# Kernel optimization log

Hardware: AMD Instinct MI355X
Metric: run time of the kernel (lower is better)

Reference implementation:

```python
import jax, jax.numpy as jnp
import numpy as np

EMB = 1024
HEADS = 16
HEAD_DIM = EMB // HEADS

def setup_inputs() -> dict:
    key = jax.random.key(0)
    ks = jax.random.split(key, 12)
    s = 0.02
    x = jax.random.normal(ks[0], (2, 2048, EMB), dtype=jnp.float32)
    return {
        "x": x,
        "wq": jax.random.normal(ks[1], (EMB, EMB), jnp.float32) * s,
        "bq": jnp.zeros((EMB,), jnp.float32),
        "wk": jax.random.normal(ks[2], (EMB, EMB), jnp.float32) * s,
        "bk": jnp.zeros((EMB,), jnp.float32),
        "wv": jax.random.normal(ks[3], (EMB, EMB), jnp.float32) * s,
        "bv": jnp.zeros((EMB,), jnp.float32),
        "wo": jax.random.normal(ks[4], (EMB, EMB), jnp.float32) * s,
        "bo": jnp.zeros((EMB,), jnp.float32),
        "gamma": jnp.ones((EMB,), jnp.float32),
        "beta": jnp.zeros((EMB,), jnp.float32),
    }

def _layernorm(x, gamma, beta, eps=1e-5):
    mu = jnp.mean(x, axis=-1, keepdims=True)
    var = jnp.mean(jnp.square(x - mu), axis=-1, keepdims=True)
    return (x - mu) * jax.lax.rsqrt(var + eps) * gamma + beta

def reference(x, wq, bq, wk, bk, wv, bv, wo, bo, gamma, beta):
    B, T, D = x.shape
    H, d_k = HEADS, HEAD_DIM
    # Linear(y = x W^T + b), then split heads
    q = (x @ wq.T + bq).reshape(B, T, H, d_k)
    k = (x @ wk.T + bk).reshape(B, T, H, d_k)
    v = (x @ wv.T + bv).reshape(B, T, H, d_k)
    scores = jnp.einsum('bthd,bshd->bhts', q, k) / jnp.sqrt(jnp.float32(d_k))
    attn = jax.nn.softmax(scores, axis=-1)  # dropout is identity in eval mode
    out = jnp.einsum('bhts,bshd->bthd', attn, v).reshape(B, T, D)
    out = out @ wo.T + bo
    return _layernorm(x + out, gamma, beta)
```

## Files before the change

### kernel.cpp

```cpp
#include <hip/hip_runtime.h>
#include <stdint.h>
#include <stddef.h>


typedef __bf16 bf16_t;
typedef bf16_t bf16x8 __attribute__((ext_vector_type(8)));
typedef float f32x16 __attribute__((ext_vector_type(16)));
typedef uint16_t u16x8 __attribute__((ext_vector_type(8)));

#define MFMA32(a, b, c) __builtin_amdgcn_mfma_f32_32x32x16_bf16((a), (b), (c), 0, 0, 0)

__device__ __forceinline__ uint16_t f2bf(float f) {
  __bf16 h = (__bf16)f;
  return *(uint16_t*)&h;
}

__device__ __forceinline__ void gload16(const void* g, void* l) {
  __builtin_amdgcn_global_load_lds((const __attribute__((address_space(1))) void*)g,
                                   (__attribute__((address_space(3))) void*)l,
                                   16, 0, 0);
}

__global__ __launch_bounds__(256) void cvt_all(
    const float* __restrict__ x, const float* __restrict__ wq,
    const float* __restrict__ wk, const float* __restrict__ wv,
    const float* __restrict__ wo, uint16_t* __restrict__ xb,
    uint16_t* __restrict__ wqb, uint16_t* __restrict__ wkb,
    uint16_t* __restrict__ wvb, uint16_t* __restrict__ wob) {
  const int gid = blockIdx.x * 256 + threadIdx.x;
  const float* src; uint16_t* dst; int off;
  if (gid < 1048576) {
    src = x; dst = xb; off = gid;
  } else {
    const int t = gid - 1048576;
    off = t & 262143;
    switch (t >> 18) {
      case 0: src = wq; dst = wqb; break;
      case 1: src = wk; dst = wkb; break;
      case 2: src = wv; dst = wvb; break;
      default: src = wo; dst = wob; break;
    }
  }
  const float4 f = ((const float4*)src)[off];
  uint64_t p = (uint64_t)f2bf(f.x) | ((uint64_t)f2bf(f.y) << 16) |
               ((uint64_t)f2bf(f.z) << 32) | ((uint64_t)f2bf(f.w) << 48);
  ((uint64_t*)dst)[off] = p;
}

template <bool OUT_BF16>
__device__ __forceinline__ void gemm128(const uint16_t* __restrict__ A,
                                        const uint16_t* __restrict__ Bt,
                                        const float* __restrict__ bias,
                                        float oscale,
                                        uint16_t* __restrict__ outb,
                                        float* __restrict__ outf) {
  __shared__ uint16_t sA[2][128 * 32];
  __shared__ uint16_t sB[2][128 * 32];
  const int tid = threadIdx.x;
  const int lane = tid & 63, w = tid >> 6;
  const int l31 = lane & 31, half = lane >> 5;
  const int m0 = blockIdx.y * 128, n0 = blockIdx.x * 128;
  const int wm = (w >> 1) * 64, wn = (w & 1) * 64;

  const int ch0 = tid, ch1 = tid + 256;
  const int r0 = ch0 >> 2, g0 = (((ch0 & 3) ^ (r0 & 3)) << 3);
  const int r1 = ch1 >> 2, g1 = (((ch1 & 3) ^ (r1 & 3)) << 3);
  const uint16_t* a0 = A + (size_t)(m0 + r0) * 1024 + g0;
  const uint16_t* a1 = A + (size_t)(m0 + r1) * 1024 + g1;
  const uint16_t* b0 = Bt + (size_t)(n0 + r0) * 1024 + g0;
  const uint16_t* b1 = Bt + (size_t)(n0 + r1) * 1024 + g1;

  gload16(a0, &sA[0][ch0 * 8]);
  gload16(a1, &sA[0][ch1 * 8]);
  gload16(b0, &sB[0][ch0 * 8]);
  gload16(b1, &sB[0][ch1 * 8]);

  f32x16 acc[2][2] = {};

  for (int kt = 0; kt < 32; ++kt) {
    __syncthreads();
    const int cur = kt & 1;
    if (kt < 31) {
      const int ko = (kt + 1) * 32;
      const int nxt = cur ^ 1;
      gload16(a0 + ko, &sA[nxt][ch0 * 8]);
      gload16(a1 + ko, &sA[nxt][ch1 * 8]);
      gload16(b0 + ko, &sB[nxt][ch0 * 8]);
      gload16(b1 + ko, &sB[nxt][ch1 * 8]);
    }
#pragma unroll
    for (int s = 0; s < 2; ++s) {
      const int c = s * 2 + half;
      bf16x8 af[2], bfr[2];
#pragma unroll
      for (int i = 0; i < 2; ++i) {
        const int arow = wm + i * 32 + l31;
        af[i] = *(const bf16x8*)&sA[cur][arow * 32 + ((c ^ (arow & 3)) << 3)];
      }
#pragma unroll
      for (int j = 0; j < 2; ++j) {
        const int brow = wn + j * 32 + l31;
        bfr[j] = *(const bf16x8*)&sB[cur][brow * 32 + ((c ^ (brow & 3)) << 3)];
      }
#pragma unroll
      for (int i = 0; i < 2; ++i)
#pragma unroll
        for (int j = 0; j < 2; ++j) acc[i][j] = MFMA32(af[i], bfr[j], acc[i][j]);
    }
  }

#pragma unroll
  for (int i = 0; i < 2; ++i) {
#pragma unroll
    for (int j = 0; j < 2; ++j) {
      const int gn = n0 + wn + j * 32 + l31;
      const float bv = bias[gn];
#pragma unroll
      for (int reg = 0; reg < 16; ++reg) {
        const int gm = m0 + wm + i * 32 + (reg & 3) + 8 * (reg >> 2) + 4 * half;
        const float v = (acc[i][j][reg] + bv) * oscale;
        const size_t idx = (size_t)gm * 1024 + gn;
        if constexpr (OUT_BF16) outb[idx] = f2bf(v);
        else outf[idx] = v;
      }
    }
  }
}

#define QSCALE 0.18033688011112042f

__global__ __launch_bounds__(256) void qkv_gemm(
    const uint16_t* __restrict__ xb, const uint16_t* __restrict__ wqb,
    const uint16_t* __restrict__ wkb, const uint16_t* __restrict__ wvb,
    const float* __restrict__ bq, const float* __restrict__ bk,
    const float* __restrict__ bv, uint16_t* __restrict__ qb,
    uint16_t* __restrict__ kb, uint16_t* __restrict__ vb) {
  const uint16_t* Bt; const float* bias; uint16_t* out; float sc;
  if (blockIdx.z == 0)      { Bt = wqb; bias = bq; out = qb; sc = QSCALE; }
  else if (blockIdx.z == 1) { Bt = wkb; bias = bk; out = kb; sc = 1.f; }
  else                      { Bt = wvb; bias = bv; out = vb; sc = 1.f; }
  gemm128<true>(xb, Bt, bias, sc, out, nullptr);
}

__global__ __launch_bounds__(256) void o_gemm(const uint16_t* __restrict__ ab,
                                              const uint16_t* __restrict__ wob,
                                              const float* __restrict__ bo,
                                              float* __restrict__ y) {
  gemm128<false>(ab, wob, bo, 1.f, nullptr, y);
}

__global__ __launch_bounds__(256) void v_trans(const uint16_t* __restrict__ vb,
                                               uint16_t* __restrict__ vbT) {
  __shared__ uint16_t sT[64 * 136];
  const int tid = threadIdx.x;
  const int t0 = blockIdx.x * 128;
  const int h = blockIdx.y, b = blockIdx.z;
#pragma unroll
  for (int c = 0; c < 4; ++c) {
    const int idx = c * 256 + tid;
    const int t = idx >> 3, d8 = (idx & 7) * 8;
    u16x8 v = *(const u16x8*)&vb[(size_t)(b * 2048 + t0 + t) * 1024 + h * 64 + d8];
#pragma unroll
    for (int e = 0; e < 8; ++e) sT[(d8 + e) * 136 + t] = v[e];
  }
  __syncthreads();
  const size_t obase = ((size_t)(b * 16 + h) * 64) * 2048 + t0;
#pragma unroll
  for (int c = 0; c < 4; ++c) {
    const int idx = c * 256 + tid;
    const int d = idx >> 4, t8 = (idx & 15) * 8;
    const int tb = t8 & ~15;
    const int add4 = (t8 & 8) ? 4 : 0;
    u16x8 v;
#pragma unroll
    for (int e = 0; e < 8; ++e)
      v[e] = sT[d * 136 + tb + ((e & 3) + ((e >> 2) << 3)) + add4];
    *(u16x8*)&vbT[obase + (size_t)d * 2048 + t8] = v;
  }
}

__global__ __launch_bounds__(512, 4) void attn(const uint16_t* __restrict__ qb,
                                               const uint16_t* __restrict__ kb,
                                               const uint16_t* __restrict__ vbT,
                                               uint16_t* __restrict__ ab) {
  __shared__ __align__(16) uint16_t smem[32768];
  uint16_t* sK = smem;
  uint16_t* sV = smem + 16384;
  const int tid = threadIdx.x;
  const int lane = tid & 63, w = tid >> 6;
  const int l31 = lane & 31, half = lane >> 5;
  const int rg = w & 3, sh = w >> 2;
  const int hb = blockIdx.x;
  const int h = hb & 15, b = hb >> 4;
  const int q0 = blockIdx.y * 128;
  const size_t qkbase = (size_t)b * 2048 * 1024 + (size_t)h * 64;
  const size_t vtbase = (size_t)hb * 64 * 2048;

  const int ch0 = tid, ch1 = tid + 512;
  const int kr0 = ch0 >> 3, kg0 = (((ch0 & 7) ^ (kr0 & 7)) << 3);
  const int kr1 = ch1 >> 3, kg1 = (((ch1 & 7) ^ (kr1 & 7)) << 3);
  const int vr0 = ch0 >> 4, vg0 = (((ch0 & 15) ^ (vr0 & 15)) << 3);
  const int vr1 = ch1 >> 4, vg1 = (((ch1 & 15) ^ (vr1 & 15)) << 3);
  const uint16_t* k0 = kb + qkbase + (size_t)kr0 * 1024 + kg0;
  const uint16_t* k1 = kb + qkbase + (size_t)kr1 * 1024 + kg1;
  const uint16_t* v0 = vbT + vtbase + (size_t)vr0 * 2048 + vg0;
  const uint16_t* v1 = vbT + vtbase + (size_t)vr1 * 2048 + vg1;

  gload16(k0, sK + ch0 * 8);
  gload16(k1, sK + ch1 * 8);
  gload16(v0, sV + ch0 * 8);
  gload16(v1, sV + ch1 * 8);

  bf16x8 qa[4];
  {
    const uint16_t* qrow =
        qb + qkbase + (size_t)(q0 + rg * 32 + l31) * 1024 + half * 8;
#pragma unroll
    for (int s4 = 0; s4 < 4; ++s4) qa[s4] = *(const bf16x8*)(qrow + s4 * 16);
  }

  f32x16 acc_o[2] = {};
  float li = 0.f;

  for (int kt = 0; kt < 16; ++kt) {
    __syncthreads();
    const int cur = kt & 1;
    if (kt < 15) {
      const size_t soK = (size_t)(kt + 1) * 128 * 1024;
      const int soV = (kt + 1) * 128;
      const int nxt = cur ^ 1;
      gload16(k0 + soK, sK + nxt * 8192 + ch0 * 8);
      gload16(k1 + soK, sK + nxt * 8192 + ch1 * 8);
      gload16(v0 + soV, sV + nxt * 8192 + ch0 * 8);
      gload16(v1 + soV, sV + nxt * 8192 + ch1 * 8);
    }
    const uint16_t* sKc = sK + cur * 8192;
    const uint16_t* sVc = sV + cur * 8192;

#pragma unroll
    for (int mblk = 0; mblk < 2; ++mblk) {
      f32x16 accs = {};
#pragma unroll
      for (int s4 = 0; s4 < 4; ++s4) {
        const int c = s4 * 2 + half;
        const int srow = sh * 64 + mblk * 32 + l31;
        const bf16x8 kk =
            *(const bf16x8*)&sKc[srow * 64 + ((c ^ (srow & 7)) << 3)];
        accs = MFMA32(kk, qa[s4], accs);
      }
      bf16x8 bp0, bp1;
#pragma unroll
      for (int reg = 0; reg < 8; ++reg) {
        const float p = __builtin_amdgcn_exp2f(accs[reg]);
        li += p;
        bp0[reg] = (__bf16)p;
      }
#pragma unroll
      for (int reg = 8; reg < 16; ++reg) {
        const float p = __builtin_amdgcn_exp2f(accs[reg]);
        li += p;
        bp1[reg - 8] = (__bf16)p;
      }
#pragma unroll
      for (int t = 0; t < 2; ++t) {
        const bf16x8 bp = t ? bp1 : bp0;
        const int cc = sh * 8 + mblk * 4 + t * 2 + half;
#pragma unroll
        for (int md = 0; md < 2; ++md) {
          const int vrow = md * 32 + l31;
          const bf16x8 vv =
              *(const bf16x8*)&sVc[vrow * 128 + ((cc ^ (vrow & 15)) << 3)];
          acc_o[md] = MFMA32(vv, bp, acc_o[md]);
        }
      }
    }
  }

  __syncthreads();
  float* ep = (float*)smem;
  float* epl = (float*)(smem + 16384);
  if (sh == 1) {
#pragma unroll
    for (int md = 0; md < 2; ++md)
#pragma unroll
      for (int reg = 0; reg < 16; ++reg)
        ep[((rg * 2 + md) * 16 + reg) * 64 + lane] = acc_o[md][reg];
    epl[rg * 64 + lane] = li;
  }
  __syncthreads();
  if (sh == 0) {
#pragma unroll
    for (int md = 0; md < 2; ++md)
#pragma unroll
      for (int reg = 0; reg < 16; ++reg)
        acc_o[md][reg] += ep[((rg * 2 + md) * 16 + reg) * 64 + lane];
    li += epl[rg * 64 + lane];
    li += __shfl_xor(li, 32);
    const float inv = 1.f / li;
    const int row = q0 + rg * 32 + l31;
    uint16_t* const obase = ab + (size_t)(b * 2048 + row) * 1024 + h * 64;
#pragma unroll
    for (int md = 0; md < 2; ++md)
#pragma unroll
      for (int g = 0; g < 4; ++g) {
        uint64_t pk = 0;
#pragma unroll
        for (int e = 0; e < 4; ++e)
          pk |= (uint64_t)f2bf(acc_o[md][g * 4 + e] * inv) << (16 * e);
        *(uint64_t*)(obase + md * 32 + g * 8 + half * 4) = pk;
      }
  }
}

__global__ __launch_bounds__(256) void resid_ln(const float* __restrict__ x,
                                                const float* __restrict__ y,
                                                const float* __restrict__ gamma,
                                                const float* __restrict__ beta,
                                                float* __restrict__ out) {
  const int row = blockIdx.x, tid = threadIdx.x;
  const size_t base = (size_t)row * 1024 + tid * 4;
  const float4 xv = *(const float4*)(x + base);
  const float4 yv = *(const float4*)(y + base);
  const float a = xv.x + yv.x, b2 = xv.y + yv.y, c = xv.z + yv.z, d = xv.w + yv.w;
  float s = a + b2 + c + d;
#pragma unroll
  for (int o = 1; o < 64; o <<= 1) s += __shfl_xor(s, o);
  __shared__ float red[4];
  const int w = tid >> 6;
  if ((tid & 63) == 0) red[w] = s;
  __syncthreads();
  const float mu = (red[0] + red[1] + red[2] + red[3]) * (1.f / 1024.f);
  const float da = a - mu, db = b2 - mu, dc = c - mu, dd = d - mu;
  float sq = da * da + db * db + dc * dc + dd * dd;
#pragma unroll
  for (int o = 1; o < 64; o <<= 1) sq += __shfl_xor(sq, o);
  __syncthreads();
  if ((tid & 63) == 0) red[w] = sq;
  __syncthreads();
  const float var = (red[0] + red[1] + red[2] + red[3]) * (1.f / 1024.f);
  const float rs = rsqrtf(var + 1e-5f);
  const float4 g = *(const float4*)(gamma + tid * 4);
  const float4 bt = *(const float4*)(beta + tid * 4);
  float4 o4;
  o4.x = da * rs * g.x + bt.x;
  o4.y = db * rs * g.y + bt.y;
  o4.z = dc * rs * g.z + bt.z;
  o4.w = dd * rs * g.w + bt.w;
  *(float4*)(out + base) = o4;
}

extern "C" void kernel_launch(void* const* d_in, const int* in_sizes, int n_in,
                              void* d_out, int out_size, void* d_ws, size_t ws_size,
                              hipStream_t stream) {
  const float* x     = (const float*)d_in[0];
  const float* wq    = (const float*)d_in[1];
  const float* bq    = (const float*)d_in[2];
  const float* wk    = (const float*)d_in[3];
  const float* bk    = (const float*)d_in[4];
  const float* wv    = (const float*)d_in[5];
  const float* bv    = (const float*)d_in[6];
  const float* wo    = (const float*)d_in[7];
  const float* bo    = (const float*)d_in[8];
  const float* gamma = (const float*)d_in[9];
  const float* beta  = (const float*)d_in[10];
  float* out = (float*)d_out;
  char* ws = (char*)d_ws;
  const size_t MB = 1024 * 1024;
  uint16_t* xb  = (uint16_t*)(ws);
  uint16_t* ab  = xb;
  uint16_t* wqb = (uint16_t*)(ws + 8 * MB);
  uint16_t* wkb = (uint16_t*)(ws + 10 * MB);
  uint16_t* wvb = (uint16_t*)(ws + 12 * MB);
  uint16_t* wob = (uint16_t*)(ws + 14 * MB);
  uint16_t* qb  = (uint16_t*)(ws + 16 * MB);
  uint16_t* kb  = (uint16_t*)(ws + 24 * MB);
  uint16_t* vb  = (uint16_t*)(ws + 32 * MB);
  uint16_t* vbT = (uint16_t*)(ws + 40 * MB);
  float*    y   = (float*)(ws + 16 * MB);

  cvt_all<<<8192, 256, 0, stream>>>(x, wq, wk, wv, wo, xb, wqb, wkb, wvb, wob);
  qkv_gemm<<<dim3(8, 32, 3), 256, 0, stream>>>(xb, wqb, wkb, wvb, bq, bk, bv, qb, kb, vb);
  v_trans<<<dim3(16, 16, 2), 256, 0, stream>>>(vb, vbT);
  attn<<<dim3(32, 16), 512, 0, stream>>>(qb, kb, vbT, ab);
  o_gemm<<<dim3(8, 32), 256, 0, stream>>>(ab, wob, bo, y);
  resid_ln<<<4096, 256, 0, stream>>>(x, y, gamma, beta, out);
}
```

Baseline: 207.9 us.

## Compute V transposed directly in QKV GEMM and use one-wave-per-row layernorm

The V projection is now computed as Wv·x^T inside the QKV GEMM, so its output lands directly in the permuted, transposed layout the attention kernel expects. This removes the separate v_trans kernel and its extra read and write of V. The residual layernorm also changes to process one row per wavefront with 4 rows per block, which drops the LDS reductions and block barriers. The transposed epilogue writes scattered 2-byte stores along rows, which may coalesce poorly.

```diff
diff --git a/kernel.cpp b/kernel.cpp
--- a/kernel.cpp
+++ b/kernel.cpp
@@ -47,19 +47,18 @@
   ((uint64_t*)dst)[off] = p;
 }
 
-template <bool OUT_BF16>
 __device__ __forceinline__ void gemm128(const uint16_t* __restrict__ A,
                                         const uint16_t* __restrict__ Bt,
                                         const float* __restrict__ bias,
                                         float oscale,
                                         uint16_t* __restrict__ outb,
-                                        float* __restrict__ outf) {
+                                        float* __restrict__ outf,
+                                        int m0, int n0, int mode) {
   __shared__ uint16_t sA[2][128 * 32];
   __shared__ uint16_t sB[2][128 * 32];
   const int tid = threadIdx.x;
   const int lane = tid & 63, w = tid >> 6;
   const int l31 = lane & 31, half = lane >> 5;
-  const int m0 = blockIdx.y * 128, n0 = blockIdx.x * 128;
   const int wm = (w >> 1) * 64, wn = (w & 1) * 64;
 
   const int ch0 = tid, ch1 = tid + 256;
@@ -109,19 +108,37 @@
     }
   }
 
-#pragma unroll
-  for (int i = 0; i < 2; ++i) {
-#pragma unroll
-    for (int j = 0; j < 2; ++j) {
-      const int gn = n0 + wn + j * 32 + l31;
-      const float bv = bias[gn];
-#pragma unroll
-      for (int reg = 0; reg < 16; ++reg) {
-        const int gm = m0 + wm + i * 32 + (reg & 3) + 8 * (reg >> 2) + 4 * half;
-        const float v = (acc[i][j][reg] + bv) * oscale;
-        const size_t idx = (size_t)gm * 1024 + gn;
-        if constexpr (OUT_BF16) outb[idx] = f2bf(v);
-        else outf[idx] = v;
+  if (mode == 2) {
+#pragma unroll
+    for (int i = 0; i < 2; ++i) {
+#pragma unroll
+      for (int j = 0; j < 2; ++j) {
+        const int gn = n0 + wn + j * 32 + l31;
+        const int bb = gn >> 11, t2 = gn & 2047;
+        const int ts = (t2 & ~12) | ((t2 & 4) << 1) | ((t2 & 8) >> 1);
+#pragma unroll
+        for (int reg = 0; reg < 16; ++reg) {
+          const int gm = m0 + wm + i * 32 + (reg & 3) + 8 * (reg >> 2) + 4 * half;
+          const float v = acc[i][j][reg] + bias[gm];
+          outb[((size_t)(bb * 1024 + gm)) * 2048 + ts] = f2bf(v);
+        }
+      }
+    }
+  } else {
+#pragma unroll
+    for (int i = 0; i < 2; ++i) {
+#pragma unroll
+      for (int j = 0; j < 2; ++j) {
+        const int gn = n0 + wn + j * 32 + l31;
+        const float bv = bias[gn];
+#pragma unroll
+        for (int reg = 0; reg < 16; ++reg) {
+          const int gm = m0 + wm + i * 32 + (reg & 3) + 8 * (reg >> 2) + 4 * half;
+          const float v = (acc[i][j][reg] + bv) * oscale;
+          const size_t idx = (size_t)gm * 1024 + gn;
+          if (mode == 0) outb[idx] = f2bf(v);
+          else outf[idx] = v;
+        }
       }
     }
   }
@@ -134,49 +151,27 @@
     const uint16_t* __restrict__ wkb, const uint16_t* __restrict__ wvb,
     const float* __restrict__ bq, const float* __restrict__ bk,
     const float* __restrict__ bv, uint16_t* __restrict__ qb,
-    uint16_t* __restrict__ kb, uint16_t* __restrict__ vb) {
-  const uint16_t* Bt; const float* bias; uint16_t* out; float sc;
-  if (blockIdx.z == 0)      { Bt = wqb; bias = bq; out = qb; sc = QSCALE; }
-  else if (blockIdx.z == 1) { Bt = wkb; bias = bk; out = kb; sc = 1.f; }
-  else                      { Bt = wvb; bias = bv; out = vb; sc = 1.f; }
-  gemm128<true>(xb, Bt, bias, sc, out, nullptr);
+    uint16_t* __restrict__ kb, uint16_t* __restrict__ vbT) {
+  const uint16_t *Aa, *Bb; const float* bias; uint16_t* out; float sc;
+  int m0, n0, mode;
+  if (blockIdx.z == 0) {
+    Aa = xb; Bb = wqb; bias = bq; out = qb; sc = QSCALE;
+    m0 = blockIdx.y * 128; n0 = blockIdx.x * 128; mode = 0;
+  } else if (blockIdx.z == 1) {
+    Aa = xb; Bb = wkb; bias = bk; out = kb; sc = 1.f;
+    m0 = blockIdx.y * 128; n0 = blockIdx.x * 128; mode = 0;
+  } else {
+    Aa = wvb; Bb = xb; bias = bv; out = vbT; sc = 1.f;
+    m0 = blockIdx.x * 128; n0 = blockIdx.y * 128; mode = 2;
+  }
+  gemm128(Aa, Bb, bias, sc, out, nullptr, m0, n0, mode);
 }
 
 __global__ __launch_bounds__(256) void o_gemm(const uint16_t* __restrict__ ab,
                                               const uint16_t* __restrict__ wob,
                                               const float* __restrict__ bo,
                                               float* __restrict__ y) {
-  gemm128<false>(ab, wob, bo, 1.f, nullptr, y);
-}
-
-__global__ __launch_bounds__(256) void v_trans(const uint16_t* __restrict__ vb,
-                                               uint16_t* __restrict__ vbT) {
-  __shared__ uint16_t sT[64 * 136];
-  const int tid = threadIdx.x;
-  const int t0 = blockIdx.x * 128;
-  const int h = blockIdx.y, b = blockIdx.z;
-#pragma unroll
-  for (int c = 0; c < 4; ++c) {
-    const int idx = c * 256 + tid;
-    const int t = idx >> 3, d8 = (idx & 7) * 8;
-    u16x8 v = *(const u16x8*)&vb[(size_t)(b * 2048 + t0 + t) * 1024 + h * 64 + d8];
-#pragma unroll
-    for (int e = 0; e < 8; ++e) sT[(d8 + e) * 136 + t] = v[e];
-  }
-  __syncthreads();
-  const size_t obase = ((size_t)(b * 16 + h) * 64) * 2048 + t0;
-#pragma unroll
-  for (int c = 0; c < 4; ++c) {
-    const int idx = c * 256 + tid;
-    const int d = idx >> 4, t8 = (idx & 15) * 8;
-    const int tb = t8 & ~15;
-    const int add4 = (t8 & 8) ? 4 : 0;
-    u16x8 v;
-#pragma unroll
-    for (int e = 0; e < 8; ++e)
-      v[e] = sT[d * 136 + tb + ((e & 3) + ((e >> 2) << 3)) + add4];
-    *(u16x8*)&vbT[obase + (size_t)d * 2048 + t8] = v;
-  }
+  gemm128(ab, wob, bo, 1.f, nullptr, y, blockIdx.y * 128, blockIdx.x * 128, 1);
 }
 
 __global__ __launch_bounds__(512, 4) void attn(const uint16_t* __restrict__ qb,
@@ -317,36 +312,49 @@
                                                 const float* __restrict__ gamma,
                                                 const float* __restrict__ beta,
                                                 float* __restrict__ out) {
-  const int row = blockIdx.x, tid = threadIdx.x;
-  const size_t base = (size_t)row * 1024 + tid * 4;
-  const float4 xv = *(const float4*)(x + base);
-  const float4 yv = *(const float4*)(y + base);
-  const float a = xv.x + yv.x, b2 = xv.y + yv.y, c = xv.z + yv.z, d = xv.w + yv.w;
-  float s = a + b2 + c + d;
+  const int tid = threadIdx.x;
+  const int lane = tid & 63, w = tid >> 6;
+  const int row = blockIdx.x * 4 + w;
+  const float* xr = x + (size_t)row * 1024;
+  const float* yr = y + (size_t)row * 1024;
+  float4 v4[4];
+  float s = 0.f;
+#pragma unroll
+  for (int t = 0; t < 4; ++t) {
+    const int off = lane * 4 + t * 256;
+    const float4 xv = *(const float4*)(xr + off);
+    const float4 yv = *(const float4*)(yr + off);
+    v4[t].x = xv.x + yv.x;
+    v4[t].y = xv.y + yv.y;
+    v4[t].z = xv.z + yv.z;
+    v4[t].w = xv.w + yv.w;
+    s += v4[t].x + v4[t].y + v4[t].z + v4[t].w;
+  }
 #pragma unroll
   for (int o = 1; o < 64; o <<= 1) s += __shfl_xor(s, o);
-  __shared__ float red[4];
-  const int w = tid >> 6;
-  if ((tid & 63) == 0) red[w] = s;
-  __syncthreads();
-  const float mu = (red[0] + red[1] + red[2] + red[3]) * (1.f / 1024.f);
-  const float da = a - mu, db = b2 - mu, dc = c - mu, dd = d - mu;
-  float sq = da * da + db * db + dc * dc + dd * dd;
+  const float mu = s * (1.f / 1024.f);
+  float sq = 0.f;
+#pragma unroll
+  for (int t = 0; t < 4; ++t) {
+    v4[t].x -= mu; v4[t].y -= mu; v4[t].z -= mu; v4[t].w -= mu;
+    sq += v4[t].x * v4[t].x + v4[t].y * v4[t].y +
+          v4[t].z * v4[t].z + v4[t].w * v4[t].w;
+  }
 #pragma unroll
   for (int o = 1; o < 64; o <<= 1) sq += __shfl_xor(sq, o);
-  __syncthreads();
-  if ((tid & 63) == 0) red[w] = sq;
-  __syncthreads();
-  const float var = (red[0] + red[1] + red[2] + red[3]) * (1.f / 1024.f);
-  const float rs = rsqrtf(var + 1e-5f);
-  const float4 g = *(const float4*)(gamma + tid * 4);
-  const float4 bt = *(const float4*)(beta + tid * 4);
-  float4 o4;
-  o4.x = da * rs * g.x + bt.x;
-  o4.y = db * rs * g.y + bt.y;
-  o4.z = dc * rs * g.z + bt.z;
-  o4.w = dd * rs * g.w + bt.w;
-  *(float4*)(out + base) = o4;
+  const float rs = rsqrtf(sq * (1.f / 1024.f) + 1e-5f);
+#pragma unroll
+  for (int t = 0; t < 4; ++t) {
+    const int off = lane * 4 + t * 256;
+    const float4 g = *(const float4*)(gamma + off);
+    const float4 bt = *(const float4*)(beta + off);
+    float4 o4;
+    o4.x = v4[t].x * rs * g.x + bt.x;
+    o4.y = v4[t].y * rs * g.y + bt.y;
+    o4.z = v4[t].z * rs * g.z + bt.z;
+    o4.w = v4[t].w * rs * g.w + bt.w;
+    *(float4*)(out + (size_t)row * 1024 + off) = o4;
+  }
 }
 
 extern "C" void kernel_launch(void* const* d_in, const int* in_sizes, int n_in,
@@ -374,14 +382,12 @@
   uint16_t* wob = (uint16_t*)(ws + 14 * MB);
   uint16_t* qb  = (uint16_t*)(ws + 16 * MB);
   uint16_t* kb  = (uint16_t*)(ws + 24 * MB);
-  uint16_t* vb  = (uint16_t*)(ws + 32 * MB);
   uint16_t* vbT = (uint16_t*)(ws + 40 * MB);
   float*    y   = (float*)(ws + 16 * MB);
 
   cvt_all<<<8192, 256, 0, stream>>>(x, wq, wk, wv, wo, xb, wqb, wkb, wvb, wob);
-  qkv_gemm<<<dim3(8, 32, 3), 256, 0, stream>>>(xb, wqb, wkb, wvb, bq, bk, bv, qb, kb, vb);
-  v_trans<<<dim3(16, 16, 2), 256, 0, stream>>>(vb, vbT);
+  qkv_gemm<<<dim3(8, 32, 3), 256, 0, stream>>>(xb, wqb, wkb, wvb, bq, bk, bv, qb, kb, vbT);
   attn<<<dim3(32, 16), 512, 0, stream>>>(qb, kb, vbT, ab);
   o_gemm<<<dim3(8, 32), 256, 0, stream>>>(ab, wob, bo, y);
-  resid_ln<<<4096, 256, 0, stream>>>(x, y, gamma, beta, out);
-}
+  resid_ln<<<1024, 256, 0, stream>>>(x, y, gamma, beta, out);
+}
```

Result: slower. 229.6 us (+10.4%).
